# Kernel tuning notes

Hardware: AMD Instinct MI355X
Metric: run time of the kernel (lower is better)

The kernel has to match this reference:

```python
import jax, jax.numpy as jnp
import numpy as np

B, D_IN, H, L, K, E, NL = 16384, 768, 1024, 128, 8192, 128, 3
CC = 0.25  # commitment cost
sg = jax.lax.stop_gradient


def _ln(x, g, b):
    # torch nn.LayerNorm, eps=1e-5
    m = jnp.mean(x, -1, keepdims=True)
    v = jnp.mean((x - m) ** 2, -1, keepdims=True)
    return (x - m) / jnp.sqrt(v + 1e-5) * g + b


def setup_inputs() -> dict:
    key = jax.random.key(0)
    ks = iter(jax.random.split(key, 32))
    def n(sh, s=0.02):
        return jax.random.normal(next(ks), sh, jnp.float32) * s
    return dict(
        x=jax.random.normal(next(ks), (B, D_IN), jnp.float32),
        eps=jax.random.normal(next(ks), (B, L), jnp.float32),
        enc_w1=n((D_IN, H)), enc_b1=jnp.zeros((H,), jnp.float32),
        enc_w2=n((H, H)), enc_b2=jnp.zeros((H,), jnp.float32),
        enc_w3=n((H, H)), enc_b3=jnp.zeros((H,), jnp.float32),
        mu_w=n((H, L)), mu_b=jnp.zeros((L,), jnp.float32),
        var_w=n((H, L)), var_b=jnp.zeros((L,), jnp.float32),
        dec_w1=n((L, H)), dec_b1=jnp.zeros((H,), jnp.float32),
        dec_w2=n((H, H)), dec_b2=jnp.zeros((H,), jnp.float32),
        dec_w3=n((H, D_IN)), dec_b3=jnp.zeros((D_IN,), jnp.float32),
        ln_g=jnp.ones((NL, L), jnp.float32),
        ln_b=jnp.zeros((NL, L), jnp.float32),
        q_in_w=n((NL, L, E)), q_in_b=jnp.zeros((NL, E), jnp.float32),
        codebook=jax.random.uniform(next(ks), (NL, K, E), jnp.float32,
                                    -1.0 / K, 1.0 / K),
        q_out_w=n((NL, E, L)), q_out_b=jnp.zeros((NL, L), jnp.float32),
    )


def reference(x, eps, enc_w1, enc_b1, enc_w2, enc_b2, enc_w3, enc_b3,
              mu_w, mu_b, var_w, var_b,
              dec_w1, dec_b1, dec_w2, dec_b2, dec_w3, dec_b3,
              ln_g, ln_b, q_in_w, q_in_b, codebook, q_out_w, q_out_b):
    # encoder MLP
    h = jax.nn.relu(x @ enc_w1 + enc_b1)
    h = jax.nn.relu(h @ enc_w2 + enc_b2)
    h = h @ enc_w3 + enc_b3
    mu = h @ mu_w + mu_b
    log_var = h @ var_w + var_b
    z = mu + eps * jnp.exp(0.5 * log_var)  # reparameterize

    # residual quantization over NL layers
    cur = z
    quantized = jnp.zeros_like(z)
    total_loss = jnp.float32(0.0)
    for i in range(NL):  # small fixed layer count
        nr = _ln(cur, ln_g[i], ln_b[i])                  # [B, L]
        f = nr @ q_in_w[i] + q_in_b[i]                   # [B, E]
        cb = codebook[i]                                 # [K, E]
        d = (jnp.sum(f * f, axis=1, keepdims=True)
             + jnp.sum(cb * cb, axis=1)
             - 2.0 * f @ cb.T)                           # [B, K]
        idx = jnp.argmin(d, axis=1)                      # [B]
        q = cb[idx] @ q_out_w[i] + q_out_b[i]            # gather == onehot@cb
        e_loss = jnp.mean((sg(q) - nr) ** 2)
        q_loss = jnp.mean((q - sg(nr)) ** 2)
        total_loss = total_loss + q_loss + CC * e_loss
        q_st = nr + sg(q - nr)                           # straight-through
        quantized = quantized + q_st
        cur = cur - q_st

    # decoder MLP
    r = jax.nn.relu(quantized @ dec_w1 + dec_b1)
    r = jax.nn.relu(r @ dec_w2 + dec_b2)
    recon = r @ dec_w3 + dec_b3
    return recon, mu, log_var, total_loss
```

## Files before the change

### kernel.cpp

```cpp
#include <hip/hip_runtime.h>
#include <stdint.h>


typedef float   floatx4  __attribute__((ext_vector_type(4)));
typedef __bf16  bf16x8   __attribute__((ext_vector_type(8)));
typedef unsigned short ushort4v __attribute__((ext_vector_type(4)));
typedef unsigned short bfbits;

#define AS1 __attribute__((address_space(1)))
#define AS3 __attribute__((address_space(3)))

__device__ __forceinline__ bfbits f2bf(float f) {
  unsigned u = __float_as_uint(f);
  u += 0x7fffu + ((u >> 16) & 1u);
  return (bfbits)(u >> 16);
}

__device__ __forceinline__ void load_lds16(const void* g, void* l) {
  __builtin_amdgcn_global_load_lds((AS1 void*)g, (AS3 void*)l, 16, 0, 0);
}

__global__ __launch_bounds__(256) void cvt_bf16_kernel(
    const float* __restrict__ in, bfbits* __restrict__ out, long n4) {
  long i = (long)blockIdx.x * 256 + threadIdx.x;
  if (i >= n4) return;
  float4 v = ((const float4*)in)[i];
  ushort4v o = { f2bf(v.x), f2bf(v.y), f2bf(v.z), f2bf(v.w) };
  ((ushort4v*)out)[i] = o;
}

__global__ __launch_bounds__(256) void transpose_bf16_kernel(
    const float* __restrict__ W, bfbits* __restrict__ Wt, int K, int N) {
  __shared__ float t[32][33];
  const long base = (long)blockIdx.z * K * N;
  const int k0 = blockIdx.y * 32, n0 = blockIdx.x * 32;
  const int tx = threadIdx.x & 31, ty = threadIdx.x >> 5;
#pragma unroll
  for (int j = 0; j < 32; j += 8)
    t[ty + j][tx] = W[base + (long)(k0 + ty + j) * N + n0 + tx];
  __syncthreads();
#pragma unroll
  for (int j = 0; j < 32; j += 8)
    Wt[base + (long)(n0 + ty + j) * K + k0 + tx] = f2bf(t[tx][ty + j]);
}

__global__ __launch_bounds__(256) void rownorm_kernel(
    const float* __restrict__ cb, float* __restrict__ out) {
  const int wave = threadIdx.x >> 6, lane = threadIdx.x & 63;
  const long row = (long)blockIdx.x * 4 + wave;
  const float* r = cb + row * 128;
  float a = r[lane], b = r[lane + 64];
  float s = a * a + b * b;
#pragma unroll
  for (int off = 1; off < 64; off <<= 1) s += __shfl_xor(s, off);
  if (lane == 0) out[row] = s;
}

template <bool RELU, bool OUTF32, bool DUAL>
__global__ __launch_bounds__(256) void gemm_kernel(
    const bfbits* __restrict__ A, const bfbits* __restrict__ Bt,
    const float* __restrict__ bias, bfbits* __restrict__ Cb,
    float* __restrict__ Cf, float* __restrict__ Cf2, int N, int Kd) {
  __shared__ bfbits Als[128 * 64];
  __shared__ bfbits Bls[128 * 64];
  const int tid = threadIdx.x;
  const int wave = tid >> 6, lane = tid & 63;
  const int wr = wave >> 1, wc = wave & 1;
  const int row0 = blockIdx.x << 7, col0 = blockIdx.y << 7;
  const int l15 = lane & 15, l16 = lane >> 4;
  const int jrow = lane >> 3;
  const int gchunk = (lane & 7) ^ jrow;

  floatx4 acc[4][4] = {};

  for (int k0 = 0; k0 < Kd; k0 += 64) {
    __syncthreads();
#pragma unroll
    for (int j = 0; j < 4; ++j) {
      const int gi = wave * 4 + j;
      const int r = gi * 8 + jrow;
      load_lds16(A + (long)(row0 + r) * Kd + (k0 + gchunk * 8),
                 Als + gi * 512 + lane * 8);
      load_lds16(Bt + (long)(col0 + r) * Kd + (k0 + gchunk * 8),
                 Bls + gi * 512 + lane * 8);
    }
    __syncthreads();
#pragma unroll
    for (int kk = 0; kk < 2; ++kk) {
      bf16x8 af[4], bf[4];
#pragma unroll
      for (int t = 0; t < 4; ++t) {
        const int ar = wr * 64 + t * 16 + l15;
        af[t] = *(const bf16x8*)(Als + ar * 64 + (((kk * 4 + l16) ^ (ar & 7)) * 8));
        const int br = wc * 64 + t * 16 + l15;
        bf[t] = *(const bf16x8*)(Bls + br * 64 + (((kk * 4 + l16) ^ (br & 7)) * 8));
      }
#pragma unroll
      for (int i = 0; i < 4; ++i)
#pragma unroll
        for (int jn = 0; jn < 4; ++jn)
          acc[i][jn] = __builtin_amdgcn_mfma_f32_16x16x32_bf16(
              af[i], bf[jn], acc[i][jn], 0, 0, 0);
    }
  }

#pragma unroll
  for (int mt = 0; mt < 4; ++mt) {
#pragma unroll
    for (int nt = 0; nt < 4; ++nt) {
      const int col = col0 + wc * 64 + nt * 16 + l15;
      const float bv = bias[col];
      const int rowb = row0 + wr * 64 + mt * 16 + l16 * 4;
#pragma unroll
      for (int r = 0; r < 4; ++r) {
        float v = acc[mt][nt][r] + bv;
        if (RELU) v = fmaxf(v, 0.f);
        if (DUAL) {
          if (col < 128) Cf[(long)(rowb + r) * 128 + col] = v;
          else           Cf2[(long)(rowb + r) * 128 + col - 128] = v;
        } else {
          const long idx = (long)(rowb + r) * N + col;
          if (OUTF32) Cf[idx] = v; else Cb[idx] = f2bf(v);
        }
      }
    }
  }
}

template <bool OUTF32>
__global__ __launch_bounds__(256) void gemm_n128_kernel(
    const bfbits* __restrict__ A, const bfbits* __restrict__ Bt,
    const float* __restrict__ bias, bfbits* __restrict__ Cb,
    float* __restrict__ Cf) {
  __shared__ bfbits Als[64 * 64];
  __shared__ bfbits Bls[128 * 64];
  const int tid = threadIdx.x;
  const int wave = tid >> 6, lane = tid & 63;
  const int wr = wave >> 1, wc = wave & 1;
  const int row0 = blockIdx.x << 6;
  const int l15 = lane & 15, l16 = lane >> 4;
  const int jrow = lane >> 3;
  const int gchunk = (lane & 7) ^ jrow;

  floatx4 acc[2][4] = {};

  for (int k0 = 0; k0 < 128; k0 += 64) {
    __syncthreads();
    {
#pragma unroll
      for (int j = 0; j < 2; ++j) {
        const int gi = wave * 2 + j;
        const int r = gi * 8 + jrow;
        load_lds16(A + (long)(row0 + r) * 128 + (k0 + gchunk * 8),
                   Als + gi * 512 + lane * 8);
      }
#pragma unroll
      for (int j = 0; j < 4; ++j) {
        const int gi = wave * 4 + j;
        const int r = gi * 8 + jrow;
        load_lds16(Bt + (long)r * 128 + (k0 + gchunk * 8),
                   Bls + gi * 512 + lane * 8);
      }
    }
    __syncthreads();
#pragma unroll
    for (int kk = 0; kk < 2; ++kk) {
      bf16x8 af[2], bf[4];
#pragma unroll
      for (int t = 0; t < 2; ++t) {
        const int ar = wr * 32 + t * 16 + l15;
        af[t] = *(const bf16x8*)(Als + ar * 64 + (((kk * 4 + l16) ^ (ar & 7)) * 8));
      }
#pragma unroll
      for (int t = 0; t < 4; ++t) {
        const int br = wc * 64 + t * 16 + l15;
        bf[t] = *(const bf16x8*)(Bls + br * 64 + (((kk * 4 + l16) ^ (br & 7)) * 8));
      }
#pragma unroll
      for (int i = 0; i < 2; ++i)
#pragma unroll
        for (int jn = 0; jn < 4; ++jn)
          acc[i][jn] = __builtin_amdgcn_mfma_f32_16x16x32_bf16(
              af[i], bf[jn], acc[i][jn], 0, 0, 0);
    }
  }

#pragma unroll
  for (int mt = 0; mt < 2; ++mt) {
#pragma unroll
    for (int nt = 0; nt < 4; ++nt) {
      const int col = wc * 64 + nt * 16 + l15;
      const float bv = bias[col];
      const int rowb = row0 + wr * 32 + mt * 16 + l16 * 4;
#pragma unroll
      for (int r = 0; r < 4; ++r) {
        const float v = acc[mt][nt][r] + bv;
        const long idx = (long)(rowb + r) * 128 + col;
        if (OUTF32) Cf[idx] = v; else Cb[idx] = f2bf(v);
      }
    }
  }
}

__global__ __launch_bounds__(512, 2) void dist2_kernel(
    const bfbits* __restrict__ A,
    const bfbits* __restrict__ Bt,
    const float* __restrict__ cbnorm,
    int2* __restrict__ cand) {
  __shared__ alignas(16) bfbits Bls[2][128 * 128];
  const int tid = threadIdx.x;
  const int wave = tid >> 6, lane = tid & 63;
  const int wr = wave & 3, wc = wave >> 2;
  const int l15 = lane & 15, l16 = lane >> 4;
  const int row0 = blockIdx.y * 256;
  const int col0 = blockIdx.x * 2048;

  bf16x8 af[4][4];
#pragma unroll
  for (int mt = 0; mt < 4; ++mt)
#pragma unroll
    for (int s = 0; s < 4; ++s)
      af[mt][s] = *(const bf16x8*)(A + (long)(row0 + wr * 64 + mt * 16 + l15) * 128 +
                                   s * 32 + l16 * 8);

  auto stage = [&](int t, int p) {
    const bfbits* src = Bt + (long)(col0 + t * 128) * 128;
    bfbits* dst = &Bls[p][0];
#pragma unroll
    for (int q = 0; q < 4; ++q) {
      const int j = q * 512 + tid;
      const int c = j >> 4;
      const int g = (j & 15) ^ (c & 15);
      load_lds16(src + (long)c * 128 + g * 8, dst + (size_t)j * 8);
    }
  };

  stage(0, 0);

  float run_val[4][4];
  int   run_col[4][4];
#pragma unroll
  for (int mt = 0; mt < 4; ++mt)
#pragma unroll
    for (int r = 0; r < 4; ++r) { run_val[mt][r] = 3.0e38f; run_col[mt][r] = 0; }

  __syncthreads();

  for (int t = 0; t < 16; ++t) {
    const bfbits* buf = &Bls[t & 1][0];
    if (t + 1 < 16) stage(t + 1, (t + 1) & 1);

    float cn[4];
    int   colv[4];
#pragma unroll
    for (int nt = 0; nt < 4; ++nt) {
      const int cl = wc * 64 + nt * 16 + l15;
      cn[nt] = cbnorm[col0 + t * 128 + cl];
      colv[nt] = t * 128 + cl;
    }

    floatx4 acc[4][4] = {};
#pragma unroll
    for (int s = 0; s < 4; ++s) {
      bf16x8 bf[4];
#pragma unroll
      for (int nt = 0; nt < 4; ++nt) {
        const int cl = wc * 64 + nt * 16 + l15;
        bf[nt] = *(const bf16x8*)(buf + (size_t)cl * 128 +
                                  (size_t)(((s * 4 + l16) ^ l15)) * 8);
      }
#pragma unroll
      for (int mt = 0; mt < 4; ++mt)
#pragma unroll
        for (int nt = 0; nt < 4; ++nt)
          acc[mt][nt] = __builtin_amdgcn_mfma_f32_16x16x32_bf16(
              af[mt][s], bf[nt], acc[mt][nt], 0, 0, 0);
    }

#pragma unroll
    for (int mt = 0; mt < 4; ++mt)
#pragma unroll
      for (int nt = 0; nt < 4; ++nt)
#pragma unroll
        for (int r = 0; r < 4; ++r) {
          const float sc = fmaf(-2.0f, acc[mt][nt][r], cn[nt]);
          if (sc < run_val[mt][r]) { run_val[mt][r] = sc; run_col[mt][r] = colv[nt]; }
        }

    __syncthreads();
  }

#pragma unroll
  for (int mt = 0; mt < 4; ++mt)
#pragma unroll
    for (int r = 0; r < 4; ++r) {
      float v = run_val[mt][r];
      int   c = run_col[mt][r];
#pragma unroll
      for (int off = 1; off < 16; off <<= 1) {
        const float ov = __shfl_xor(v, off);
        const int   oc = __shfl_xor(c, off);
        if (ov < v || (ov == v && oc < c)) { v = ov; c = oc; }
      }
      if (l15 == 0) {
        const int row = row0 + wr * 64 + mt * 16 + l16 * 4 + r;
        cand[(long)row * 8 + blockIdx.x * 2 + wc] =
            make_int2(__float_as_int(v), col0 + c);
      }
    }
}

__global__ __launch_bounds__(256) void argmin8_kernel(
    const int2* __restrict__ cand, const float* __restrict__ cb,
    bfbits* __restrict__ cbg) {
  const int wave = threadIdx.x >> 6, lane = threadIdx.x & 63;
  const long row = (long)blockIdx.x * 4 + wave;
  float v = 3.0e38f; int k = 0x7fffffff;
  if (lane < 8) {
    int2 c = cand[row * 8 + lane];
    v = __int_as_float(c.x); k = c.y;
  }
#pragma unroll
  for (int off = 1; off < 8; off <<= 1) {
    float ov = __shfl_xor(v, off);
    int   ok = __shfl_xor(k, off);
    if (ov < v || (ov == v && ok < k)) { v = ov; k = ok; }
  }
  k = __shfl(k, 0);
  const float* src = cb + (long)k * 128;
  cbg[row * 128 + lane]      = f2bf(src[lane]);
  cbg[row * 128 + lane + 64] = f2bf(src[lane + 64]);
}

__device__ __forceinline__ void ln_row(float c0, float c1, int lane,
                                       const float* __restrict__ g,
                                       const float* __restrict__ bta,
                                       long row, bfbits* __restrict__ nrb,
                                       float* __restrict__ nrf) {
  float s = c0 + c1, sq = c0 * c0 + c1 * c1;
#pragma unroll
  for (int off = 1; off < 64; off <<= 1) {
    s += __shfl_xor(s, off);
    sq += __shfl_xor(sq, off);
  }
  const float m = s * (1.f / 128.f);
  const float var = fmaxf(sq * (1.f / 128.f) - m * m, 0.f);
  const float rstd = rsqrtf(var + 1e-5f);
  const float y0 = (c0 - m) * rstd * g[lane] + bta[lane];
  const float y1 = (c1 - m) * rstd * g[lane + 64] + bta[lane + 64];
  nrf[row * 128 + lane] = y0;
  nrf[row * 128 + lane + 64] = y1;
  nrb[row * 128 + lane] = f2bf(y0);
  nrb[row * 128 + lane + 64] = f2bf(y1);
}

__global__ __launch_bounds__(256) void reparam_ln_kernel(
    const float* __restrict__ mu, const float* __restrict__ lv,
    const float* __restrict__ eps, float* __restrict__ cur,
    float* __restrict__ qnt, const float* __restrict__ g,
    const float* __restrict__ bta, bfbits* __restrict__ nrb,
    float* __restrict__ nrf) {
  const int wave = threadIdx.x >> 6, lane = threadIdx.x & 63;
  const long row = (long)blockIdx.x * 4 + wave;
  const long i0 = row * 128 + lane, i1 = i0 + 64;
  const float z0 = mu[i0] + eps[i0] * expf(0.5f * lv[i0]);
  const float z1 = mu[i1] + eps[i1] * expf(0.5f * lv[i1]);
  cur[i0] = z0; cur[i1] = z1;
  qnt[i0] = 0.f; qnt[i1] = 0.f;
  ln_row(z0, z1, lane, g, bta, row, nrb, nrf);
}

template <bool DO_LN>
__global__ __launch_bounds__(256) void qupd_ln_kernel(
    const float* __restrict__ q, float* __restrict__ nrf,
    float* __restrict__ cur, float* __restrict__ qnt,
    const float* __restrict__ g, const float* __restrict__ bta,
    bfbits* __restrict__ nrb, float* __restrict__ lossp) {
  const int wave = threadIdx.x >> 6, lane = threadIdx.x & 63;
  const long row = (long)blockIdx.x * 4 + wave;
  const long i0 = row * 128 + lane, i1 = i0 + 64;
  const float q0 = q[i0], q1 = q[i1];
  const float d0 = q0 - nrf[i0], d1 = q1 - nrf[i1];
  qnt[i0] += q0; qnt[i1] += q1;
  float p = d0 * d0 + d1 * d1;
#pragma unroll
  for (int off = 1; off < 64; off <<= 1) p += __shfl_xor(p, off);
  __shared__ float sp[4];
  if (lane == 0) sp[wave] = p;
  __syncthreads();
  if (threadIdx.x == 0) lossp[blockIdx.x] = sp[0] + sp[1] + sp[2] + sp[3];
  if (DO_LN) {
    const float c0 = cur[i0] - q0, c1 = cur[i1] - q1;
    cur[i0] = c0; cur[i1] = c1;
    ln_row(c0, c1, lane, g, bta, row, nrb, nrf);
  }
}

__global__ __launch_bounds__(256) void loss_reduce_kernel(
    const float* __restrict__ lossp, float* __restrict__ out, int n) {
  float s = 0.f;
  for (int i = threadIdx.x; i < n; i += 256) s += lossp[i];
#pragma unroll
  for (int off = 1; off < 64; off <<= 1) s += __shfl_xor(s, off);
  __shared__ float sp[4];
  const int wave = threadIdx.x >> 6, lane = threadIdx.x & 63;
  if (lane == 0) sp[wave] = s;
  __syncthreads();
  if (threadIdx.x == 0)
    *out = (sp[0] + sp[1] + sp[2] + sp[3]) * (1.25f / 2097152.f);
}

static void launch_gemm(bool relu, bool outf32, const bfbits* A,
                        const bfbits* Bt, const float* bias, bfbits* Cb,
                        float* Cf, int M, int N, int Kd, hipStream_t s) {
  dim3 g(M / 128, N / 128), b(256);
  if (relu) {
    gemm_kernel<true, false, false><<<g, b, 0, s>>>(A, Bt, bias, Cb, Cf, nullptr, N, Kd);
  } else if (outf32) {
    gemm_kernel<false, true, false><<<g, b, 0, s>>>(A, Bt, bias, Cb, Cf, nullptr, N, Kd);
  } else {
    gemm_kernel<false, false, false><<<g, b, 0, s>>>(A, Bt, bias, Cb, Cf, nullptr, N, Kd);
  }
}

extern "C" void kernel_launch(void* const* d_in, const int* in_sizes, int n_in,
                              void* d_out, int out_size, void* d_ws,
                              size_t ws_size, hipStream_t stream) {
  (void)in_sizes; (void)n_in; (void)out_size; (void)ws_size;
  constexpr long B = 16384, DIN = 768, H = 1024, L = 128, K = 8192;

  const float* x    = (const float*)d_in[0];
  const float* eps  = (const float*)d_in[1];
  const float* ew1  = (const float*)d_in[2];
  const float* eb1  = (const float*)d_in[3];
  const float* ew2  = (const float*)d_in[4];
  const float* eb2  = (const float*)d_in[5];
  const float* ew3  = (const float*)d_in[6];
  const float* eb3  = (const float*)d_in[7];
  const float* muw  = (const float*)d_in[8];
  const float* mub  = (const float*)d_in[9];
  const float* vaw  = (const float*)d_in[10];
  const float* vab  = (const float*)d_in[11];
  const float* dw1  = (const float*)d_in[12];
  const float* db1  = (const float*)d_in[13];
  const float* dw2  = (const float*)d_in[14];
  const float* db2  = (const float*)d_in[15];
  const float* dw3  = (const float*)d_in[16];
  const float* db3  = (const float*)d_in[17];
  const float* lng  = (const float*)d_in[18];
  const float* lnb  = (const float*)d_in[19];
  const float* qinw = (const float*)d_in[20];
  const float* qinb = (const float*)d_in[21];
  const float* cb   = (const float*)d_in[22];
  const float* qow  = (const float*)d_in[23];
  const float* qob  = (const float*)d_in[24];

  float* out = (float*)d_out;
  float* out_mu   = out + B * DIN;
  float* out_lv   = out_mu + B * L;
  float* out_loss = out_lv + B * L;

  char* ws = (char*)d_ws;
  constexpr size_t O_W1T  = 0;
  constexpr size_t O_W2T  = O_W1T + 1024 * 768 * 2;
  constexpr size_t O_W3T  = O_W2T + 1024 * 1024 * 2;
  constexpr size_t O_MUT  = O_W3T + 1024 * 1024 * 2;
  constexpr size_t O_VART = O_MUT + 128 * 1024 * 2;
  constexpr size_t O_DW1T = O_VART + 128 * 1024 * 2;
  constexpr size_t O_DW2T = O_DW1T + 1024 * 128 * 2;
  constexpr size_t O_DW3T = O_DW2T + 1024 * 1024 * 2;
  constexpr size_t O_QINT = O_DW3T + 768 * 1024 * 2;
  constexpr size_t O_QOUT = O_QINT + 3 * 128 * 128 * 2;
  constexpr size_t O_CBB  = O_QOUT + 3 * 128 * 128 * 2;
  constexpr size_t O_CBN  = O_CBB + 3 * 8192 * 128 * 2;
  constexpr size_t O_B2   = O_CBN + 3 * 8192 * 4;
  constexpr size_t O_LOSSP= O_B2 + 256 * 4;
  constexpr size_t O_CUR  = O_LOSSP + 3 * 4096 * 4;
  constexpr size_t O_QNT  = O_CUR + B * L * 4;
  constexpr size_t O_NRF  = O_QNT + B * L * 4;
  constexpr size_t O_H1   = O_NRF + B * L * 4;
  constexpr size_t O_H2   = O_H1 + B * H * 2;
  constexpr size_t O_H3   = O_H2 + B * H * 2;
  constexpr size_t O_NRB  = O_H2;
  constexpr size_t O_FB   = O_H2 + B * L * 2;
  constexpr size_t O_CBG  = O_H2 + 2 * B * L * 2;
  constexpr size_t O_QBUF = O_H2 + 3 * B * L * 2;
  constexpr size_t O_CAND = O_H2 + 3 * B * L * 2 + B * L * 4;
  constexpr size_t O_XB   = O_H3;
  constexpr size_t O_QZB  = O_H3;

  bfbits* w1t  = (bfbits*)(ws + O_W1T);
  bfbits* w2t  = (bfbits*)(ws + O_W2T);
  bfbits* w3t  = (bfbits*)(ws + O_W3T);
  bfbits* mut  = (bfbits*)(ws + O_MUT);
  bfbits* vart = (bfbits*)(ws + O_VART);
  bfbits* dw1t = (bfbits*)(ws + O_DW1T);
  bfbits* dw2t = (bfbits*)(ws + O_DW2T);
  bfbits* dw3t = (bfbits*)(ws + O_DW3T);
  bfbits* qint = (bfbits*)(ws + O_QINT);
  bfbits* qout = (bfbits*)(ws + O_QOUT);
  bfbits* cbb  = (bfbits*)(ws + O_CBB);
  float*  cbn  = (float*)(ws + O_CBN);
  float*  bias2= (float*)(ws + O_B2);
  float*  lossp= (float*)(ws + O_LOSSP);
  float*  cur  = (float*)(ws + O_CUR);
  float*  qnt  = (float*)(ws + O_QNT);
  float*  nrf  = (float*)(ws + O_NRF);
  bfbits* h1   = (bfbits*)(ws + O_H1);
  bfbits* h2   = (bfbits*)(ws + O_H2);
  bfbits* h3   = (bfbits*)(ws + O_H3);
  bfbits* nrb  = (bfbits*)(ws + O_NRB);
  bfbits* fb   = (bfbits*)(ws + O_FB);
  bfbits* cbg  = (bfbits*)(ws + O_CBG);
  float*  qbuf = (float*)(ws + O_QBUF);
  int2*   cand = (int2*)(ws + O_CAND);
  bfbits* xb   = (bfbits*)(ws + O_XB);
  bfbits* qzb  = (bfbits*)(ws + O_QZB);
  bfbits* r1   = h1;
  bfbits* r2   = h2;

  cvt_bf16_kernel<<<dim3((B * DIN) / 4 / 256), dim3(256), 0, stream>>>(x, xb, (B * DIN) / 4);
  cvt_bf16_kernel<<<dim3((3 * K * 128) / 4 / 256), dim3(256), 0, stream>>>(cb, cbb, (3 * K * 128) / 4);
  transpose_bf16_kernel<<<dim3(1024 / 32, 768 / 32, 1), dim3(256), 0, stream>>>(ew1, w1t, 768, 1024);
  transpose_bf16_kernel<<<dim3(32, 32, 1), dim3(256), 0, stream>>>(ew2, w2t, 1024, 1024);
  transpose_bf16_kernel<<<dim3(32, 32, 1), dim3(256), 0, stream>>>(ew3, w3t, 1024, 1024);
  transpose_bf16_kernel<<<dim3(128 / 32, 32, 1), dim3(256), 0, stream>>>(muw, mut, 1024, 128);
  transpose_bf16_kernel<<<dim3(128 / 32, 32, 1), dim3(256), 0, stream>>>(vaw, vart, 1024, 128);
  transpose_bf16_kernel<<<dim3(32, 128 / 32, 1), dim3(256), 0, stream>>>(dw1, dw1t, 128, 1024);
  transpose_bf16_kernel<<<dim3(32, 32, 1), dim3(256), 0, stream>>>(dw2, dw2t, 1024, 1024);
  transpose_bf16_kernel<<<dim3(768 / 32, 32, 1), dim3(256), 0, stream>>>(dw3, dw3t, 1024, 768);
  transpose_bf16_kernel<<<dim3(4, 4, 3), dim3(256), 0, stream>>>(qinw, qint, 128, 128);
  transpose_bf16_kernel<<<dim3(4, 4, 3), dim3(256), 0, stream>>>(qow, qout, 128, 128);
  rownorm_kernel<<<dim3(3 * K / 4), dim3(256), 0, stream>>>(cb, cbn);
  hipMemcpyAsync(bias2, mub, 128 * 4, hipMemcpyDeviceToDevice, stream);
  hipMemcpyAsync(bias2 + 128, vab, 128 * 4, hipMemcpyDeviceToDevice, stream);

  launch_gemm(true, false, xb, w1t, eb1, h1, nullptr, B, 1024, 768, stream);
  launch_gemm(true, false, h1, w2t, eb2, h2, nullptr, B, 1024, 1024, stream);
  launch_gemm(false, false, h2, w3t, eb3, h3, nullptr, B, 1024, 1024, stream);
  gemm_kernel<false, true, true><<<dim3(128, 2), dim3(256), 0, stream>>>(
      h3, mut, bias2, nullptr, out_mu, out_lv, 256, 1024);

  reparam_ln_kernel<<<dim3(B / 4), dim3(256), 0, stream>>>(
      out_mu, out_lv, eps, cur, qnt, lng, lnb, nrb, nrf);

  for (int i = 0; i < 3; ++i) {
    gemm_n128_kernel<false><<<dim3(B / 64), dim3(256), 0, stream>>>(
        nrb, qint + (size_t)i * 128 * 128, qinb + i * 128, fb, nullptr);
    dist2_kernel<<<dim3(4, 64), dim3(512), 0, stream>>>(
        fb, cbb + (size_t)i * K * 128, cbn + (size_t)i * K, cand);
    argmin8_kernel<<<dim3(B / 4), dim3(256), 0, stream>>>(
        cand, cb + (size_t)i * K * 128, cbg);
    gemm_n128_kernel<true><<<dim3(B / 64), dim3(256), 0, stream>>>(
        cbg, qout + (size_t)i * 128 * 128, qob + i * 128, nullptr, qbuf);
    if (i < 2) {
      qupd_ln_kernel<true><<<dim3(B / 4), dim3(256), 0, stream>>>(
          qbuf, nrf, cur, qnt, lng + (i + 1) * 128, lnb + (i + 1) * 128,
          nrb, lossp + (size_t)i * 4096);
    } else {
      qupd_ln_kernel<false><<<dim3(B / 4), dim3(256), 0, stream>>>(
          qbuf, nrf, cur, qnt, nullptr, nullptr, nullptr,
          lossp + (size_t)i * 4096);
    }
  }
  loss_reduce_kernel<<<dim3(1), dim3(256), 0, stream>>>(lossp, out_loss, 3 * 4096);

  cvt_bf16_kernel<<<dim3((B * L) / 4 / 256), dim3(256), 0, stream>>>(qnt, qzb, (B * L) / 4);
  launch_gemm(true, false, qzb, dw1t, db1, r1, nullptr, B, 1024, 128, stream);
  launch_gemm(true, false, r1, dw2t, db2, r2, nullptr, B, 1024, 1024, stream);
  launch_gemm(false, true, r2, dw3t, db3, nullptr, out, B, 768, 1024, stream);
}
```

Baseline: 666.2 us.

## Add 256x256-tile double-buffered MFMA GEMM for the large encoder/decoder layers

Adds a new GEMM kernel with 256x256 output tiles, 512 threads, double-buffered LDS staging via global_load_lds, interleaved prefetch within the k-loop, s_setprio around MFMA bursts, and an XCD-aware block swizzle. It replaces the 128x128 GEMM for the five large encoder and decoder matmuls, aiming for more operand reuse per LDS byte and better overlap of memory traffic with MFMA work. The costs are 128KB of LDS per block, high register pressure from 32 accumulators, and fewer blocks in flight (e.g. 256 blocks for N=1024).

```diff
diff --git a/kernel.cpp b/kernel.cpp
--- a/kernel.cpp
+++ b/kernel.cpp
@@ -127,6 +127,174 @@
   }
 }
 
+template <bool RELU, bool OUTF32>
+__global__ __launch_bounds__(512, 2) void gemm256_kernel(
+    const bfbits* __restrict__ A, const bfbits* __restrict__ Bt,
+    const float* __restrict__ bias, bfbits* __restrict__ Cb,
+    float* __restrict__ Cf, int N, int Kd) {
+  __shared__ alignas(16) bfbits As[2][256 * 64];
+  __shared__ alignas(16) bfbits Bs[2][256 * 64];
+  const int tid = threadIdx.x;
+  const int w = tid >> 6, lane = tid & 63;
+  const int wr = w >> 2, wc = w & 3;
+  const int l15 = lane & 15, l16 = lane >> 4;
+  const int jrow = lane >> 3;
+  const int gch = (lane & 7) ^ jrow;
+
+  const int nbx = gridDim.x, nby = gridDim.y;
+  const int nwg = nbx * nby;
+  const int cpx = nwg >> 3;
+  const int lid = blockIdx.y * nbx + blockIdx.x;
+  const int swz = (lid & 7) * cpx + (lid >> 3);
+  const int bm = swz / nby, bn = swz % nby;
+  const long row0 = (long)bm << 8;
+  const long col0 = (long)bn << 8;
+
+  const int NT = Kd >> 6;
+
+  auto stageA = [&](int t, int hh) {
+    const bfbits* src = A + (row0 + hh * 128) * Kd + t * 64 + gch * 8;
+    bfbits* dst = &As[t & 1][hh * 8192];
+#pragma unroll
+    for (int q = 0; q < 2; ++q) {
+      const int gi = q * 8 + w;
+      load_lds16(src + (long)(gi * 8 + jrow) * Kd, dst + gi * 512 + lane * 8);
+    }
+  };
+  auto stageB = [&](int t, int hh) {
+    const bfbits* src = Bt + (col0 + hh * 128) * Kd + t * 64 + gch * 8;
+    bfbits* dst = &Bs[t & 1][hh * 8192];
+#pragma unroll
+    for (int q = 0; q < 2; ++q) {
+      const int gi = q * 8 + w;
+      load_lds16(src + (long)(gi * 8 + jrow) * Kd, dst + gi * 512 + lane * 8);
+    }
+  };
+
+  auto rdA = [&](int p, int i, int kk) -> bf16x8 {
+    const int r = wr * 128 + i * 16 + l15;
+    return *(const bf16x8*)(&As[p][r * 64 + (((kk * 4 + l16) ^ (r & 7)) * 8)]);
+  };
+  auto rdB = [&](int p, int j, int kk) -> bf16x8 {
+    const int r = wc * 64 + j * 16 + l15;
+    return *(const bf16x8*)(&Bs[p][r * 64 + (((kk * 4 + l16) ^ (r & 7)) * 8)]);
+  };
+
+  floatx4 acc[8][4] = {};
+
+  stageA(0, 0); stageA(0, 1); stageB(0, 0); stageB(0, 1);
+  stageA(1, 0);
+  asm volatile("s_waitcnt vmcnt(2)" ::: "memory");
+  __builtin_amdgcn_s_barrier();
+
+  for (int s = 0; s < NT; ++s) {
+    const int p = s & 1;
+    bf16x8 bfr[4];
+
+    {
+      bf16x8 af[4];
+#pragma unroll
+      for (int t = 0; t < 4; ++t) af[t] = rdA(p, t, 0);
+#pragma unroll
+      for (int t = 0; t < 4; ++t) bfr[t] = rdB(p, t, 0);
+      if (s + 1 < NT) stageA(s + 1, 1);
+      __builtin_amdgcn_s_barrier();
+      asm volatile("s_waitcnt lgkmcnt(0)" ::: "memory");
+      __builtin_amdgcn_sched_barrier(0);
+      __builtin_amdgcn_s_setprio(1);
+#pragma unroll
+      for (int i = 0; i < 4; ++i)
+#pragma unroll
+        for (int j = 0; j < 4; ++j)
+          acc[i][j] = __builtin_amdgcn_mfma_f32_16x16x32_bf16(
+              af[i], bfr[j], acc[i][j], 0, 0, 0);
+      __builtin_amdgcn_s_setprio(0);
+      __builtin_amdgcn_s_barrier();
+    }
+    {
+      bf16x8 af[4];
+#pragma unroll
+      for (int t = 0; t < 4; ++t) af[t] = rdA(p, 4 + t, 0);
+      if (s + 1 < NT) stageB(s + 1, 0);
+      __builtin_amdgcn_s_barrier();
+      asm volatile("s_waitcnt lgkmcnt(0)" ::: "memory");
+      __builtin_amdgcn_sched_barrier(0);
+      __builtin_amdgcn_s_setprio(1);
+#pragma unroll
+      for (int i = 0; i < 4; ++i)
+#pragma unroll
+        for (int j = 0; j < 4; ++j)
+          acc[4 + i][j] = __builtin_amdgcn_mfma_f32_16x16x32_bf16(
+              af[i], bfr[j], acc[4 + i][j], 0, 0, 0);
+      __builtin_amdgcn_s_setprio(0);
+      __builtin_amdgcn_s_barrier();
+    }
+    {
+      bf16x8 af[4];
+#pragma unroll
+      for (int t = 0; t < 4; ++t) af[t] = rdA(p, t, 1);
+#pragma unroll
+      for (int t = 0; t < 4; ++t) bfr[t] = rdB(p, t, 1);
+      if (s + 1 < NT) stageB(s + 1, 1);
+      __builtin_amdgcn_s_barrier();
+      asm volatile("s_waitcnt lgkmcnt(0)" ::: "memory");
+      __builtin_amdgcn_sched_barrier(0);
+      __builtin_amdgcn_s_setprio(1);
+#pragma unroll
+      for (int i = 0; i < 4; ++i)
+#pragma unroll
+        for (int j = 0; j < 4; ++j)
+          acc[i][j] = __builtin_amdgcn_mfma_f32_16x16x32_bf16(
+              af[i], bfr[j], acc[i][j], 0, 0, 0);
+      __builtin_amdgcn_s_setprio(0);
+      __builtin_amdgcn_s_barrier();
+    }
+    {
+      bf16x8 af[4];
+#pragma unroll
+      for (int t = 0; t < 4; ++t) af[t] = rdA(p, 4 + t, 1);
+      __builtin_amdgcn_s_barrier();
+      asm volatile("s_waitcnt lgkmcnt(0)" ::: "memory");
+      __builtin_amdgcn_sched_barrier(0);
+      __builtin_amdgcn_s_setprio(1);
+#pragma unroll
+      for (int i = 0; i < 4; ++i)
+#pragma unroll
+        for (int j = 0; j < 4; ++j)
+          acc[4 + i][j] = __builtin_amdgcn_mfma_f32_16x16x32_bf16(
+              af[i], bfr[j], acc[4 + i][j], 0, 0, 0);
+      __builtin_amdgcn_s_setprio(0);
+      __builtin_amdgcn_s_barrier();
+    }
+    if (s + 1 < NT) {
+      if (s + 2 < NT) {
+        stageA(s + 2, 0);
+        asm volatile("s_waitcnt vmcnt(2)" ::: "memory");
+      } else {
+        asm volatile("s_waitcnt vmcnt(0)" ::: "memory");
+      }
+      __builtin_amdgcn_s_barrier();
+    }
+  }
+
+#pragma unroll
+  for (int i = 0; i < 8; ++i) {
+    const long rowb = row0 + wr * 128 + i * 16 + l16 * 4;
+#pragma unroll
+    for (int j = 0; j < 4; ++j) {
+      const int col = (int)col0 + wc * 64 + j * 16 + l15;
+      const float bv = bias[col];
+#pragma unroll
+      for (int r = 0; r < 4; ++r) {
+        float v = acc[i][j][r] + bv;
+        if (RELU) v = fmaxf(v, 0.f);
+        const long idx = (rowb + r) * N + col;
+        if (OUTF32) Cf[idx] = v; else Cb[idx] = f2bf(v);
+      }
+    }
+  }
+}
+
 template <bool OUTF32>
 __global__ __launch_bounds__(256) void gemm_n128_kernel(
     const bfbits* __restrict__ A, const bfbits* __restrict__ Bt,
@@ -420,6 +588,19 @@
     gemm_kernel<false, true, false><<<g, b, 0, s>>>(A, Bt, bias, Cb, Cf, nullptr, N, Kd);
   } else {
     gemm_kernel<false, false, false><<<g, b, 0, s>>>(A, Bt, bias, Cb, Cf, nullptr, N, Kd);
+  }
+}
+
+static void launch_gemm256(bool relu, bool outf32, const bfbits* A,
+                           const bfbits* Bt, const float* bias, bfbits* Cb,
+                           float* Cf, int M, int N, int Kd, hipStream_t s) {
+  dim3 g(M / 256, N / 256), b(512);
+  if (relu) {
+    gemm256_kernel<true, false><<<g, b, 0, s>>>(A, Bt, bias, Cb, Cf, N, Kd);
+  } else if (outf32) {
+    gemm256_kernel<false, true><<<g, b, 0, s>>>(A, Bt, bias, Cb, Cf, N, Kd);
+  } else {
+    gemm256_kernel<false, false><<<g, b, 0, s>>>(A, Bt, bias, Cb, Cf, N, Kd);
   }
 }
 
@@ -535,9 +716,9 @@
   hipMemcpyAsync(bias2, mub, 128 * 4, hipMemcpyDeviceToDevice, stream);
   hipMemcpyAsync(bias2 + 128, vab, 128 * 4, hipMemcpyDeviceToDevice, stream);
 
-  launch_gemm(true, false, xb, w1t, eb1, h1, nullptr, B, 1024, 768, stream);
-  launch_gemm(true, false, h1, w2t, eb2, h2, nullptr, B, 1024, 1024, stream);
-  launch_gemm(false, false, h2, w3t, eb3, h3, nullptr, B, 1024, 1024, stream);
+  launch_gemm256(true, false, xb, w1t, eb1, h1, nullptr, B, 1024, 768, stream);
+  launch_gemm256(true, false, h1, w2t, eb2, h2, nullptr, B, 1024, 1024, stream);
+  launch_gemm256(false, false, h2, w3t, eb3, h3, nullptr, B, 1024, 1024, stream);
   gemm_kernel<false, true, true><<<dim3(128, 2), dim3(256), 0, stream>>>(
       h3, mut, bias2, nullptr, out_mu, out_lv, 256, 1024);
 
@@ -567,6 +748,6 @@
 
   cvt_bf16_kernel<<<dim3((B * L) / 4 / 256), dim3(256), 0, stream>>>(qnt, qzb, (B * L) / 4);
   launch_gemm(true, false, qzb, dw1t, db1, r1, nullptr, B, 1024, 128, stream);
-  launch_gemm(true, false, r1, dw2t, db2, r2, nullptr, B, 1024, 1024, stream);
-  launch_gemm(false, true, r2, dw3t, db3, nullptr, out, B, 768, 1024, stream);
-}
+  launch_gemm256(true, false, r1, dw2t, db2, r2, nullptr, B, 1024, 1024, stream);
+  launch_gemm256(false, true, r2, dw3t, db3, nullptr, out, B, 768, 1024, stream);
+}
```

Result: no change. 663.2 us (-0.5%).
